# Kernel optimization log

Hardware: AMD Instinct MI355X
Metric: run time of the kernel (lower is better)

The kernel has to match this reference:

```python
import jax, jax.numpy as jnp
import numpy as np

K = 1024  # num_embeddings
D = 256   # embedding_dim
COMMIT = 0.25

def setup_inputs() -> dict:
    key = jax.random.key(0)
    k1, k2 = jax.random.split(key)
    z = jax.random.normal(k1, (32, 256, 32, 32), dtype=jnp.float32)
    # matches nn.Embedding init uniform_(-1/K, 1/K)
    emb = jax.random.uniform(k2, (K, D), dtype=jnp.float32, minval=-1.0 / K, maxval=1.0 / K)
    return {"z": z, "emb": emb}

def reference(z, emb):
    B, C, H, W = z.shape
    zp = jnp.transpose(z, (0, 2, 3, 1))            # (B,H,W,C)
    z_flat = zp.reshape(-1, C)                      # (N,D)
    # squared euclidean distances (N,K)
    d = (jnp.sum(z_flat * z_flat, axis=1, keepdims=True)
         + jnp.sum(emb * emb, axis=1)
         - 2.0 * z_flat @ emb.T)
    idx = jnp.argmin(d, axis=1)                     # (N,)
    quantized_flat = emb[idx]                       # gather == one-hot @ emb
    quantized = quantized_flat.reshape(zp.shape)    # (B,H,W,C)
    e_latent_loss = jnp.mean((jax.lax.stop_gradient(quantized) - zp) ** 2)
    q_latent_loss = jnp.mean((quantized - jax.lax.stop_gradient(zp)) ** 2)
    loss = q_latent_loss + COMMIT * e_latent_loss
    # straight-through estimator
    quantized_st = zp + jax.lax.stop_gradient(quantized - zp)
    # perplexity: avg one-hot probs == normalized counts
    N = z_flat.shape[0]
    counts = jnp.zeros((K,), dtype=jnp.float32).at[idx].add(1.0)
    avg_probs = counts / N
    perplexity = jnp.exp(-jnp.sum(avg_probs * jnp.log(avg_probs + 1e-10)))
    out = jnp.transpose(quantized_st, (0, 3, 1, 2))  # (B,C,H,W)
    return (out, loss, perplexity)
```

## Files before the change

kernel.cpp:

```cpp
#include <hip/hip_runtime.h>
#include <math.h>

#define KC 1024
#define DD 256
#define NROWS 32768
#define NELEM 8388608

typedef _Float16 f16;
typedef __attribute__((ext_vector_type(8))) _Float16 f16x8;
typedef __attribute__((ext_vector_type(16))) float f32x16;

#define KEY_SCALE 2097152.0f
#define KEY_INV   (1.0f / 2097152.0f)

__global__ void vq_prep_kernel(const float* __restrict__ emb, f16* __restrict__ emb_h,
                               float* __restrict__ c_sq, int* __restrict__ counts,
                               float* __restrict__ loss_acc, unsigned* __restrict__ done) {
    const int tid = threadIdx.x;
    const int gt = blockIdx.x * 256 + tid;
    if (gt < KC) counts[gt] = 0;
    if (gt == 0) { *loss_acc = 0.0f; *done = 0u; }
    {
        int k = blockIdx.x * 4 + (tid >> 6);
        int lane = tid & 63;
        float4 v = *(const float4*)(emb + (size_t)k * DD + lane * 4);
        float s = v.x * v.x + v.y * v.y + v.z * v.z + v.w * v.w;
        #pragma unroll
        for (int off = 32; off > 0; off >>= 1) s += __shfl_down(s, off);
        if (lane == 0) c_sq[k] = s;
    }
    if (gt < 32768) {
        int code = gt & 1023;
        int kg = gt >> 10;
        const float* p = emb + (size_t)code * DD + kg * 8;
        float4 v0 = *(const float4*)p;
        float4 v1 = *(const float4*)(p + 4);
        f16x8 h;
        h[0] = (f16)v0.x; h[1] = (f16)v0.y; h[2] = (f16)v0.z; h[3] = (f16)v0.w;
        h[4] = (f16)v1.x; h[5] = (f16)v1.y; h[6] = (f16)v1.z; h[7] = (f16)v1.w;
        *(f16x8*)(emb_h + (size_t)gt * 8) = h;
    }
}

__global__ __launch_bounds__(512, 4)
void vq_main_kernel(const float* __restrict__ z, const float* __restrict__ emb,
                    const f16* __restrict__ emb_h, const float* __restrict__ c_sq,
                    int* __restrict__ counts, float* __restrict__ loss_acc,
                    unsigned* __restrict__ done, float* __restrict__ out,
                    float* __restrict__ out_tail) {
    __shared__ __align__(16) char smem_raw[66560];
    __shared__ int   bl_key[8][64];
    __shared__ float zsq_part[8][64];
    __shared__ int   idx_s[64];
    __shared__ float wsum[8];
    __shared__ int   last_flag;

    f16* z_s = (f16*)smem_raw;
    float* Qh = (float*)smem_raw;

    const int tid = threadIdx.x;
    const int n0 = blockIdx.x * 64;
    const int b = n0 >> 10;
    const int hw0 = n0 & 1023;

    {
        const int r = tid & 63;
        const int kq = tid >> 6;
        const float* zp = z + (size_t)b * (DD * 1024) + hw0 + r;
        float sq = 0.f;
        #pragma unroll
        for (int it = 0; it < 4; ++it) {
            int kg = kq * 4 + it;
            f16x8 hv;
            #pragma unroll
            for (int j = 0; j < 8; ++j) {
                float v = zp[(size_t)(kg * 8 + j) * 1024];
                sq += v * v;
                hv[j] = (f16)v;
            }
            *(f16x8*)&z_s[(kg * 64 + r) * 8] = hv;
        }
        zsq_part[kq][r] = sq;
    }
    __syncthreads();

    const int m = tid & 31;
    const int h = (tid >> 5) & 1;
    const int w = tid >> 6;

    int bk[32];
    #pragma unroll
    for (int s = 0; s < 32; ++s) bk[s] = 0x7FFFFFFF;

    for (int c = 0; c < 4; ++c) {
        const int cb = w * 128 + c * 32;
        const int code = cb + m;
        const f16* ebp = emb_h + (size_t)h * 8192 + (size_t)code * 8;

        f32x16 acc0, acc1;
        #pragma unroll
        for (int i = 0; i < 16; ++i) { acc0[i] = 0.f; acc1[i] = 0.f; }

        #pragma unroll 4
        for (int ks = 0; ks < 16; ++ks) {
            const f16* za = z_s + (2 * ks + h) * 512 + m * 8;
            f16x8 a0 = *(const f16x8*)(za);
            f16x8 a1 = *(const f16x8*)(za + 256);
            f16x8 b0 = *(const f16x8*)(ebp + (size_t)ks * 16384);
            acc0 = __builtin_amdgcn_mfma_f32_32x32x16_f16(a0, b0, acc0, 0, 0, 0);
            acc1 = __builtin_amdgcn_mfma_f32_32x32x16_f16(a1, b0, acc1, 0, 0, 0);
        }

        const float cs = c_sq[code];
        #pragma unroll
        for (int reg = 0; reg < 16; ++reg) {
            float s0 = fmaf(-2.f, acc0[reg], cs);
            float s1 = fmaf(-2.f, acc1[reg], cs);
            int k0 = (int)(s0 * KEY_SCALE) * 1024 + code;
            int k1 = (int)(s1 * KEY_SCALE) * 1024 + code;
            bk[reg] = min(bk[reg], k0);
            bk[16 + reg] = min(bk[16 + reg], k1);
        }
    }

    #pragma unroll
    for (int s = 0; s < 32; ++s) {
        int k = bk[s];
        #pragma unroll
        for (int d = 16; d >= 1; d >>= 1) k = min(k, __shfl_xor(k, d));
        bk[s] = k;
    }
    if (m == 0) {
        #pragma unroll
        for (int s = 0; s < 32; ++s) {
            int rt = s >> 4, reg = s & 15;
            int row = rt * 32 + (reg & 3) + 8 * (reg >> 2) + 4 * h;
            bl_key[w][row] = bk[s];
        }
    }
    __syncthreads();

    if (tid < 64) {
        int k = bl_key[0][tid];
        #pragma unroll
        for (int w2 = 1; w2 < 8; ++w2) k = min(k, bl_key[w2][tid]);
        int i = k & 1023;
        idx_s[tid] = i;
        atomicAdd(&counts[i], 1);
        float zq = 0.f;
        #pragma unroll
        for (int p = 0; p < 8; ++p) zq += zsq_part[p][tid];
        float lr = (float)(k >> 10) * KEY_INV + zq;
        #pragma unroll
        for (int off = 32; off > 0; off >>= 1) lr += __shfl_down(lr, off);
        if (tid == 0) atomicAdd(loss_acc, lr);
    }
    __syncthreads();

    {
        int r = tid & 63;
        int part = tid >> 6;
        const float* ep = emb + (size_t)idx_s[r] * DD + part * 32;
        float* qrow = Qh + r * 260 + part * 32;
        #pragma unroll
        for (int g = 0; g < 8; ++g)
            *(float4*)(qrow + g * 4) = *(const float4*)(ep + g * 4);
    }
    __syncthreads();

    {
        int r = tid & 63;
        const float* qr = Qh + r * 260;
        const size_t base = (size_t)b * (DD * 1024) + hw0 + r;
        #pragma unroll
        for (int g = 0; g < 8; ++g) {
            int c0 = w * 32 + g * 4;
            float4 v = *(const float4*)(qr + c0);
            out[base + (size_t)c0 * 1024] = v.x;
            out[base + (size_t)(c0 + 1) * 1024] = v.y;
            out[base + (size_t)(c0 + 2) * 1024] = v.z;
            out[base + (size_t)(c0 + 3) * 1024] = v.w;
        }
    }

    __syncthreads();
    if (tid == 0) {
        __threadfence();
        last_flag = (atomicAdd(done, 1u) == 511u) ? 1 : 0;
    }
    __syncthreads();
    if (last_flag) {
        __threadfence();
        float s = 0.f;
        for (int k = tid; k < KC; k += 512) {
            int cnt = atomicAdd(&counts[k], 0);
            float p = (float)cnt * (1.0f / (float)NROWS);
            s += p * logf(p + 1e-10f);
        }
        #pragma unroll
        for (int off = 32; off > 0; off >>= 1) s += __shfl_down(s, off);
        if ((tid & 63) == 0) wsum[w] = s;
        __syncthreads();
        if (tid == 0) {
            float ent = 0.f;
            #pragma unroll
            for (int p = 0; p < 8; ++p) ent += wsum[p];
            float ls = atomicAdd(loss_acc, 0.0f);
            out_tail[0] = 1.25f * ls * (1.0f / (float)NELEM);
            out_tail[1] = expf(-ent);
        }
    }
}

extern "C" void kernel_launch(void* const* d_in, const int* in_sizes, int n_in,
                              void* d_out, int out_size, void* d_ws, size_t ws_size,
                              hipStream_t stream) {
    const float* z = (const float*)d_in[0];
    const float* emb = (const float*)d_in[1];
    float* out = (float*)d_out;

    char* wsb = (char*)d_ws;
    f16* emb_h = (f16*)wsb;
    float* c_sq = (float*)(wsb + 524288);
    int* counts = (int*)(wsb + 528384);
    float* loss_acc = (float*)(wsb + 532480);
    unsigned* done = (unsigned*)(wsb + 532484);

    hipLaunchKernelGGL(vq_prep_kernel, dim3(256), dim3(256), 0, stream,
                       emb, emb_h, c_sq, counts, loss_acc, done);
    hipLaunchKernelGGL(vq_main_kernel, dim3(512), dim3(512), 0, stream,
                       z, emb, emb_h, c_sq, counts, loss_acc, done, out, out + NELEM);
}
```

Before: 132.5 us.

## Prefetch codebook fragments into registers and write output via register transpose

The MFMA inner loop now keeps a four-deep ring of B-operand fragments in registers. Each iteration issues the load for four steps ahead, across chunk boundaries, so global codebook latency overlaps the matrix ops. The gathered-embedding output stage no longer stages through a 66KB LDS buffer. Each thread loads 4 rows of 8 channels, transposes them in registers and writes float4 stores along the spatial dimension. This cuts LDS use and one barrier, but adds register pressure at 512 threads with launch bounds of 4 blocks.

After: 184.3 us. 39.1% more time.

```diff
diff --git a/kernel.cpp b/kernel.cpp
--- a/kernel.cpp
+++ b/kernel.cpp
@@ -48,20 +48,23 @@
                     int* __restrict__ counts, float* __restrict__ loss_acc,
                     unsigned* __restrict__ done, float* __restrict__ out,
                     float* __restrict__ out_tail) {
-    __shared__ __align__(16) char smem_raw[66560];
+    __shared__ __align__(16) f16 z_s[16384];
     __shared__ int   bl_key[8][64];
     __shared__ float zsq_part[8][64];
     __shared__ int   idx_s[64];
     __shared__ float wsum[8];
     __shared__ int   last_flag;
 
-    f16* z_s = (f16*)smem_raw;
-    float* Qh = (float*)smem_raw;
-
     const int tid = threadIdx.x;
     const int n0 = blockIdx.x * 64;
     const int b = n0 >> 10;
     const int hw0 = n0 & 1023;
+
+    const int m = tid & 31;
+    const int h = (tid >> 5) & 1;
+    const int w = tid >> 6;
+
+    const f16* ebase = emb_h + (size_t)h * 8192 + (size_t)(w * 128 + m) * 8;
 
     {
         const int r = tid & 63;
@@ -82,33 +85,37 @@
         }
         zsq_part[kq][r] = sq;
     }
-    __syncthreads();
-
-    const int m = tid & 31;
-    const int h = (tid >> 5) & 1;
-    const int w = tid >> 6;
+
+    f16x8 bF[4];
+    #pragma unroll
+    for (int p = 0; p < 4; ++p) bF[p] = *(const f16x8*)(ebase + (size_t)p * 16384);
+
+    __syncthreads();
 
     int bk[32];
     #pragma unroll
     for (int s = 0; s < 32; ++s) bk[s] = 0x7FFFFFFF;
 
     for (int c = 0; c < 4; ++c) {
-        const int cb = w * 128 + c * 32;
-        const int code = cb + m;
-        const f16* ebp = emb_h + (size_t)h * 8192 + (size_t)code * 8;
+        const int code = w * 128 + c * 32 + m;
 
         f32x16 acc0, acc1;
         #pragma unroll
         for (int i = 0; i < 16; ++i) { acc0[i] = 0.f; acc1[i] = 0.f; }
 
-        #pragma unroll 4
+        #pragma unroll
         for (int ks = 0; ks < 16; ++ks) {
+            f16x8 bcur = bF[ks & 3];
+            {
+                const int pf = ks + 4;
+                bF[ks & 3] = *(const f16x8*)(ebase + (size_t)(c + (pf >> 4)) * 256
+                                                   + (size_t)(pf & 15) * 16384);
+            }
             const f16* za = z_s + (2 * ks + h) * 512 + m * 8;
             f16x8 a0 = *(const f16x8*)(za);
             f16x8 a1 = *(const f16x8*)(za + 256);
-            f16x8 b0 = *(const f16x8*)(ebp + (size_t)ks * 16384);
-            acc0 = __builtin_amdgcn_mfma_f32_32x32x16_f16(a0, b0, acc0, 0, 0, 0);
-            acc1 = __builtin_amdgcn_mfma_f32_32x32x16_f16(a1, b0, acc1, 0, 0, 0);
+            acc0 = __builtin_amdgcn_mfma_f32_32x32x16_f16(a0, bcur, acc0, 0, 0, 0);
+            acc1 = __builtin_amdgcn_mfma_f32_32x32x16_f16(a1, bcur, acc1, 0, 0, 0);
         }
 
         const float cs = c_sq[code];
@@ -158,28 +165,29 @@
     __syncthreads();
 
     {
-        int r = tid & 63;
-        int part = tid >> 6;
-        const float* ep = emb + (size_t)idx_s[r] * DD + part * 32;
-        float* qrow = Qh + r * 260 + part * 32;
-        #pragma unroll
-        for (int g = 0; g < 8; ++g)
-            *(float4*)(qrow + g * 4) = *(const float4*)(ep + g * 4);
-    }
-    __syncthreads();
-
-    {
-        int r = tid & 63;
-        const float* qr = Qh + r * 260;
-        const size_t base = (size_t)b * (DD * 1024) + hw0 + r;
-        #pragma unroll
-        for (int g = 0; g < 8; ++g) {
-            int c0 = w * 32 + g * 4;
-            float4 v = *(const float4*)(qr + c0);
-            out[base + (size_t)c0 * 1024] = v.x;
-            out[base + (size_t)(c0 + 1) * 1024] = v.y;
-            out[base + (size_t)(c0 + 2) * 1024] = v.z;
-            out[base + (size_t)(c0 + 3) * 1024] = v.w;
+        const int rgrp = tid & 15;
+        const int cg = tid >> 4;
+        float4 e0[4], e1[4];
+        #pragma unroll
+        for (int i = 0; i < 4; ++i) {
+            const float* ep = emb + (size_t)idx_s[rgrp * 4 + i] * DD + cg * 8;
+            e0[i] = *(const float4*)ep;
+            e1[i] = *(const float4*)(ep + 4);
+        }
+        const size_t base = (size_t)b * (DD * 1024) + hw0 + rgrp * 4;
+        #pragma unroll
+        for (int j = 0; j < 4; ++j) {
+            float4 st;
+            st.x = (&e0[0].x)[j]; st.y = (&e0[1].x)[j];
+            st.z = (&e0[2].x)[j]; st.w = (&e0[3].x)[j];
+            *(float4*)(out + base + (size_t)(cg * 8 + j) * 1024) = st;
+        }
+        #pragma unroll
+        for (int j = 0; j < 4; ++j) {
+            float4 st;
+            st.x = (&e1[0].x)[j]; st.y = (&e1[1].x)[j];
+            st.z = (&e1[2].x)[j]; st.w = (&e1[3].x)[j];
+            *(float4*)(out + base + (size_t)(cg * 8 + 4 + j) * 1024) = st;
         }
     }
 
```
